# Optimization experiments

Measured on AMD Instinct MI355X. Metric: run time of the kernel, lower is better.

## Reference

```python
import jax, jax.numpy as jnp
import numpy as np

EPS = 1e-6
NUM_HEADS = 16

def _ln(x):
    m = jnp.mean(x, -1, keepdims=True)
    v = jnp.mean((x - m) ** 2, -1, keepdims=True)
    return (x - m) * jax.lax.rsqrt(v + EPS)

def _rms(x, w):
    return x * jax.lax.rsqrt(jnp.mean(x * x, -1, keepdims=True) + EPS) * w

def _to_mha(t):
    B, S, D = t.shape
    return t.reshape(B, S, NUM_HEADS, D // NUM_HEADS).transpose(0, 2, 1, 3)

def _rope(t, freqs):
    # t: [B,H,T,Hd], freqs: [T, Hd//2, 2] (cos, sin)
    B, H, T, Hd = t.shape
    tr = t.reshape(B, H, T, Hd // 2, 2)
    cos, sin = freqs[..., 0], freqs[..., 1]
    r = tr[..., 0] * cos - tr[..., 1] * sin
    i = tr[..., 0] * sin + tr[..., 1] * cos
    return jnp.stack([r, i], -1).reshape(B, H, T, Hd)

def _pre(h, qk_w, qn, kn, v_w, v_b):
    qk = h @ qk_w.T                      # [B,S,2D], no bias (c_qk bias=False)
    q, k = jnp.split(qk, 2, -1)
    q = _rms(_to_mha(q), qn)             # per-head RMSNorm
    k = _rms(_to_mha(k), kn)
    v = _to_mha(h @ v_w.T + v_b)
    return q, k, v

def _post(x, a, pw, pb, w1, b1, w3, b3, w2, b2):
    x = x + a @ pw.T + pb                # residual + c_proj
    h = _ln(x)
    m = (jax.nn.silu(h @ w1.T + b1) * (h @ w3.T + b3)) @ w2.T + b2  # SwiGLU
    return x + m

def _forward(x, c, freqs, px_qk_w, px_qn, px_kn, px_v_w, px_v_b,
             pc_qk_w, pc_qn, pc_kn, pc_v_w, pc_v_b,
             p1_proj_w, p1_proj_b, p1_w1, p1_b1, p1_w3, p1_b3, p1_w2, p1_b2,
             p2_proj_w, p2_proj_b, p2_w1, p2_b1, p2_w3, p2_b3, p2_w2, p2_b2):
    x_ln, c_ln = _ln(x), _ln(c)
    qc, kc, vc = _pre(c_ln, pc_qk_w, pc_qn, pc_kn, pc_v_w, pc_v_b)
    qx, kx, vx = _pre(x_ln, px_qk_w, px_qn, px_kn, px_v_w, px_v_b)
    q = jnp.concatenate([qc, qx], 2)     # [B,H,T,Hd], T = S+L
    k = jnp.concatenate([kc, kx], 2)
    v = jnp.concatenate([vc, vx], 2)
    q = _rope(q, freqs)
    k = _rope(k, freqs)
    Hd = q.shape[-1]
    scores = jnp.einsum('bhqd,bhkd->bhqk', q, k) / jnp.sqrt(jnp.float32(Hd))
    T = scores.shape[-1]
    causal = jnp.tril(jnp.ones((T, T), bool))
    scores = jnp.where(causal, scores, jnp.finfo(scores.dtype).min)
    p = jax.nn.softmax(scores, -1)
    y = jnp.einsum('bhqk,bhkd->bhqd', p, v)
    B, D = x.shape[0], x.shape[-1]
    y = y.transpose(0, 2, 1, 3).reshape(B, -1, D)  # [B,T,D]
    S = c.shape[1]
    y_c, y_x = y[:, :S], y[:, S:]
    x_out = _post(x, y_x, p1_proj_w, p1_proj_b, p1_w1, p1_b1, p1_w3, p1_b3, p1_w2, p1_b2)
    c_out = _post(c, y_c, p2_proj_w, p2_proj_b, p2_w1, p2_b1, p2_w3, p2_b3, p2_w2, p2_b2)
    return x_out, c_out

def setup_inputs() -> dict:
    B, L, S, D, H, FF = 1, 1536, 512, 1024, 16, 4096
    Hd, T = D // H, L + S
    key = jax.random.key(0)
    ks = iter(jax.random.split(key, 40))
    def rn(shape, s=0.02):
        return (jax.random.normal(next(ks), shape, jnp.float32) * s)
    pos = jnp.arange(T, dtype=jnp.float32)
    inv = 1.0 / (10000.0 ** (jnp.arange(0, Hd, 2, dtype=jnp.float32) / Hd))
    ang = pos[:, None] * inv[None, :]
    freqs = jnp.stack([jnp.cos(ang), jnp.sin(ang)], -1)  # [T, Hd//2, 2]
    inp = {
        'x': jax.random.normal(next(ks), (B, L, D), jnp.float32),
        'c': jax.random.normal(next(ks), (B, S, D), jnp.float32),
        'freqs': freqs,
        'px_qk_w': rn((2 * D, D)), 'px_qn': jnp.ones((Hd,)), 'px_kn': jnp.ones((Hd,)),
        'px_v_w': rn((D, D)), 'px_v_b': rn((D,)),
        'pc_qk_w': rn((2 * D, D)), 'pc_qn': jnp.ones((Hd,)), 'pc_kn': jnp.ones((Hd,)),
        'pc_v_w': rn((D, D)), 'pc_v_b': rn((D,)),
    }
    for pfx in ('p1', 'p2'):
        inp[pfx + '_proj_w'] = rn((D, D)); inp[pfx + '_proj_b'] = rn((D,))
        inp[pfx + '_w1'] = rn((FF, D)); inp[pfx + '_b1'] = rn((FF,))
        inp[pfx + '_w3'] = rn((FF, D)); inp[pfx + '_b3'] = rn((FF,))
        inp[pfx + '_w2'] = rn((D, FF)); inp[pfx + '_b2'] = rn((D,))
    return inp

def reference(x, c, freqs, px_qk_w, px_qn, px_kn, px_v_w, px_v_b,
              pc_qk_w, pc_qn, pc_kn, pc_v_w, pc_v_b,
              p1_proj_w, p1_proj_b, p1_w1, p1_b1, p1_w3, p1_b3, p1_w2, p1_b2,
              p2_proj_w, p2_proj_b, p2_w1, p2_b1, p2_w3, p2_b3, p2_w2, p2_b2):
    return _forward(x, c, freqs, px_qk_w, px_qn, px_kn, px_v_w, px_v_b,
                    pc_qk_w, pc_qn, pc_kn, pc_v_w, pc_v_b,
                    p1_proj_w, p1_proj_b, p1_w1, p1_b1, p1_w3, p1_b3, p1_w2, p1_b2,
                    p2_proj_w, p2_proj_b, p2_w1, p2_b1, p2_w3, p2_b3, p2_w2, p2_b2)
```

## Files before the change

### kernel.cpp

```cpp
#include <hip/hip_runtime.h>

typedef __attribute__((ext_vector_type(8))) short short8;
typedef __attribute__((ext_vector_type(4))) float floatx4;

__device__ __forceinline__ float bf2f(unsigned short u) {
  union { unsigned int i; float f; } v; v.i = ((unsigned int)u) << 16; return v.f;
}
__device__ __forceinline__ unsigned short f2bf(float f) {
  union { float f; unsigned int i; } v; v.f = f;
  unsigned int x = v.i + 0x7fffu + ((v.i >> 16) & 1u);
  return (unsigned short)(x >> 16);
}
__device__ __forceinline__ float loadE(const void* p, size_t i, int f) {
  return f ? ((const float*)p)[i] : bf2f(((const unsigned short*)p)[i]);
}
__device__ __forceinline__ uint4 packbf(float4 a, float4 b) {
  union { unsigned short u[8]; uint4 v; } p;
  p.u[0] = f2bf(a.x); p.u[1] = f2bf(a.y); p.u[2] = f2bf(a.z); p.u[3] = f2bf(a.w);
  p.u[4] = f2bf(b.x); p.u[5] = f2bf(b.y); p.u[6] = f2bf(b.z); p.u[7] = f2bf(b.w);
  return p.v;
}

__global__ void detect_kernel(const unsigned int* __restrict__ probe, int* __restrict__ flag) {
  if (threadIdx.x == 0 && blockIdx.x == 0) *flag = (probe[0] == 0x3F800000u) ? 1 : 0;
}

struct CArgs {
  const void* in[12];
  unsigned short* out[12];
  unsigned int cum[12];
};
__global__ __launch_bounds__(256) void convw_kernel(CArgs a, int total_chunks,
                                                    const int* __restrict__ flagp) {
  const int flag = *flagp;
  for (int c = blockIdx.x * 256 + threadIdx.x; c < total_chunks; c += gridDim.x * 256) {
    int s = 0;
    while (c >= (int)a.cum[s]) ++s;
    unsigned int base = s ? a.cum[s - 1] : 0u;
    size_t e = (size_t)(c - base) * 8;
    if (flag) {
      const float* in = (const float*)a.in[s] + e;
      float4 v0 = *(const float4*)in;
      float4 v1 = *(const float4*)(in + 4);
      *(uint4*)(a.out[s] + e) = packbf(v0, v1);
    } else {
      *(uint4*)(a.out[s] + e) = *(const uint4*)((const unsigned short*)a.in[s] + e);
    }
  }
}

__global__ __launch_bounds__(256) void zero_kernel(void* __restrict__ out, int out_elems,
                                                   const int* __restrict__ flagp) {
  int limit = (*flagp) ? (out_elems >> 2) : (out_elems >> 3);
  int i = blockIdx.x * 256 + threadIdx.x;
  if (i < limit) ((uint4*)out)[i] = make_uint4(0, 0, 0, 0);
}

__global__ __launch_bounds__(256) void ln_ext_kernel(const void* __restrict__ cin,
                                                     const void* __restrict__ xin,
                                                     unsigned short* __restrict__ out,
                                                     const int* __restrict__ flagp) {
  const int D = 1024, S = 512;
  const int flag = *flagp;
  int row = blockIdx.x;
  const void* src = (row < S) ? cin : xin;
  size_t rb = (size_t)(row < S ? row : row - S) * D;
  int base = threadIdx.x * 4;
  float x0 = loadE(src, rb + base + 0, flag);
  float x1 = loadE(src, rb + base + 1, flag);
  float x2 = loadE(src, rb + base + 2, flag);
  float x3 = loadE(src, rb + base + 3, flag);
  float s1 = x0 + x1 + x2 + x3;
  float s2 = x0 * x0 + x1 * x1 + x2 * x2 + x3 * x3;
  for (int off = 32; off; off >>= 1) {
    s1 += __shfl_down(s1, off, 64);
    s2 += __shfl_down(s2, off, 64);
  }
  __shared__ float red[8];
  int wid = threadIdx.x >> 6;
  if ((threadIdx.x & 63) == 0) { red[wid] = s1; red[4 + wid] = s2; }
  __syncthreads();
  s1 = red[0] + red[1] + red[2] + red[3];
  s2 = red[4] + red[5] + red[6] + red[7];
  float mean = s1 * (1.0f / D);
  float var = s2 * (1.0f / D) - mean * mean;
  float inv = rsqrtf(var + 1e-6f);
  unsigned short* dst = out + (size_t)row * D + base;
  dst[0] = f2bf((x0 - mean) * inv);
  dst[1] = f2bf((x1 - mean) * inv);
  dst[2] = f2bf((x2 - mean) * inv);
  dst[3] = f2bf((x3 - mean) * inv);
}

__global__ __launch_bounds__(256) void ln_mid_kernel(const unsigned short* __restrict__ in,
                                                     unsigned short* __restrict__ outc,
                                                     unsigned short* __restrict__ outx) {
  const int D = 1024, S = 512;
  int row = blockIdx.x;
  const unsigned short* src = in + (size_t)row * D;
  int base = threadIdx.x * 4;
  float x0 = bf2f(src[base + 0]);
  float x1 = bf2f(src[base + 1]);
  float x2 = bf2f(src[base + 2]);
  float x3 = bf2f(src[base + 3]);
  float s1 = x0 + x1 + x2 + x3;
  float s2 = x0 * x0 + x1 * x1 + x2 * x2 + x3 * x3;
  for (int off = 32; off; off >>= 1) {
    s1 += __shfl_down(s1, off, 64);
    s2 += __shfl_down(s2, off, 64);
  }
  __shared__ float red[8];
  int wid = threadIdx.x >> 6;
  if ((threadIdx.x & 63) == 0) { red[wid] = s1; red[4 + wid] = s2; }
  __syncthreads();
  s1 = red[0] + red[1] + red[2] + red[3];
  s2 = red[4] + red[5] + red[6] + red[7];
  float mean = s1 * (1.0f / D);
  float var = s2 * (1.0f / D) - mean * mean;
  float inv = rsqrtf(var + 1e-6f);
  unsigned short* dst = (row < S ? outc + (size_t)row * D : outx + (size_t)(row - S) * D) + base;
  dst[0] = f2bf((x0 - mean) * inv);
  dst[1] = f2bf((x1 - mean) * inv);
  dst[2] = f2bf((x2 - mean) * inv);
  dst[3] = f2bf((x3 - mean) * inv);
}

struct GArgs {
  const unsigned short* A[4];
  const void* B[4];
  const void* bias[4];
  const void* res[4];
  void* C[4];
  unsigned long long oo[4];
  int mcum[4];
  int N[4];
  int K;
  int nd;
};

#define BAR() asm volatile("s_waitcnt lgkmcnt(0)\n\ts_barrier" ::: "memory")

template <int RES_MODE, int OUT_MODE, int SPLITK, int BBF16>
__global__ __launch_bounds__(256) void gemm_kernel(GArgs g, const int* __restrict__ flagp) {
  const int flag = *flagp;
  int by = blockIdx.y;
  int d = 0;
  while (d < g.nd - 1 && by >= g.mcum[d]) ++d;
  int mbase = (d == 0) ? 0 : g.mcum[d - 1];
  const int m0 = (by - mbase) * 128;
  const int N = g.N[d];
  const int n0 = blockIdx.x * 128;
  if (n0 >= N) return;
  const int K = g.K;
  int kbeg = 0, kend = K;
  if (SPLITK > 1) {
    if (!flag) {
      if (blockIdx.z != 0) return;
    } else {
      int kl = K / SPLITK;
      kbeg = blockIdx.z * kl;
      kend = kbeg + kl;
    }
  }
  const int nt = (kend - kbeg) >> 5;

  __shared__ __align__(16) unsigned short sA[2 * 5120];
  __shared__ __align__(16) unsigned short sB[2 * 5120];

  const int tid = threadIdx.x;
  const int lane = tid & 63;
  const int wave = tid >> 6;
  const int wm = (wave >> 1) * 64, wn = (wave & 1) * 64;
  const int srow = tid >> 2;
  const int scol = (tid & 3) * 8;
  const int wo0 = srow * 40 + scol;
  const int wo1 = wo0 + 64 * 40;
  const unsigned short* Ag0 = g.A[d] + (size_t)(m0 + srow) * K + kbeg + scol;
  const unsigned short* Ag1 = Ag0 + (size_t)64 * K;
  const unsigned short* Bh0 = (const unsigned short*)g.B[d] + (size_t)(n0 + srow) * K + kbeg + scol;
  const unsigned short* Bh1 = Bh0 + (size_t)64 * K;
  const float* Bf0 = (const float*)g.B[d] + (size_t)(n0 + srow) * K + kbeg + scol;
  const float* Bf1 = Bf0 + (size_t)64 * K;

  uint4 ra0, ra1, rb0, rb1;
  auto load_tile = [&](int kk) {
    ra0 = *(const uint4*)(Ag0 + kk);
    ra1 = *(const uint4*)(Ag1 + kk);
    if (BBF16 || !flag) {
      rb0 = *(const uint4*)(Bh0 + kk);
      rb1 = *(const uint4*)(Bh1 + kk);
    } else {
      float4 x0 = *(const float4*)(Bf0 + kk), x1 = *(const float4*)(Bf0 + kk + 4);
      float4 y0 = *(const float4*)(Bf1 + kk), y1 = *(const float4*)(Bf1 + kk + 4);
      rb0 = packbf(x0, x1);
      rb1 = packbf(y0, y1);
    }
  };
  auto store_tile = [&](int buf) {
    unsigned short* sa = sA + buf * 5120;
    unsigned short* sb = sB + buf * 5120;
    *(uint4*)(sa + wo0) = ra0;
    *(uint4*)(sa + wo1) = ra1;
    *(uint4*)(sb + wo0) = rb0;
    *(uint4*)(sb + wo1) = rb1;
  };

  load_tile(0);
  store_tile(0);
  if (nt > 1) load_tile(32);
  BAR();

  const int fr = lane & 15, fc = (lane >> 4) * 8;
  floatx4 acc[4][4] = {};
  for (int t = 0; t < nt; ++t) {
    if (t + 1 < nt) {
      store_tile((t + 1) & 1);
      if (t + 2 < nt) load_tile((t + 2) * 32);
    }
    const unsigned short* as = sA + (t & 1) * 5120;
    const unsigned short* bs = sB + (t & 1) * 5120;
    short8 af[4], bfr[4];
    #pragma unroll
    for (int i = 0; i < 4; ++i) {
      af[i]  = *(const short8*)(as + (wm + i * 16 + fr) * 40 + fc);
      bfr[i] = *(const short8*)(bs + (wn + i * 16 + fr) * 40 + fc);
    }
    #pragma unroll
    for (int mi = 0; mi < 4; ++mi)
      #pragma unroll
      for (int ni = 0; ni < 4; ++ni)
        acc[mi][ni] = __builtin_amdgcn_mfma_f32_16x16x32_bf16(af[mi], bfr[ni], acc[mi][ni], 0, 0, 0);
    if (t + 1 < nt) BAR();
  }

  const void* bias = g.bias[d];
  const void* res = g.res[d];
  void* C = g.C[d];
  const size_t oo = g.oo[d];
  const bool first = (SPLITK <= 1) || (blockIdx.z == 0) || !flag;
  #pragma unroll
  for (int mi = 0; mi < 4; ++mi)
    #pragma unroll
    for (int ni = 0; ni < 4; ++ni)
      #pragma unroll
      for (int r = 0; r < 4; ++r) {
        int row = m0 + wm + mi * 16 + (lane >> 4) * 4 + r;
        int col = n0 + wn + ni * 16 + (lane & 15);
        float val = acc[mi][ni][r];
        size_t off = (size_t)row * N + col;
        if (first) {
          if (bias) val += loadE(bias, (size_t)col, flag);
          if (RES_MODE == 1) val += loadE(res, off, flag);
          if (RES_MODE == 3) {
            float h1v = bf2f(((const unsigned short*)res)[off]);
            val = (h1v / (1.0f + __expf(-h1v))) * val;
          }
          if (RES_MODE == 4) val += bf2f(((const unsigned short*)res)[off]);
        }
        if (OUT_MODE == 0) {
          ((unsigned short*)C)[off] = f2bf(val);
        } else {
          if (flag) {
            if (SPLITK > 1) atomicAdd((float*)C + oo + off, val);
            else            ((float*)C)[oo + off] = val;
          } else {
            ((unsigned short*)C)[oo + off] = f2bf(val);
          }
        }
      }
}

__global__ __launch_bounds__(256) void rmsrope_kernel(
    unsigned short* __restrict__ qk,
    const void* __restrict__ qn_c, const void* __restrict__ kn_c,
    const void* __restrict__ qn_x, const void* __restrict__ kn_x,
    const void* __restrict__ freqs, const int* __restrict__ flagp) {
  const int flag = *flagp;
  int t = blockIdx.x;
  int h = blockIdx.y * 4 + (threadIdx.x >> 6);
  int d = threadIdx.x & 63;
  unsigned short* qrow = qk + (size_t)t * 2048 + h * 64;
  unsigned short* krow = qrow + 1024;
  float q = bf2f(qrow[d]), k = bf2f(krow[d]);
  float qs = q * q, ks = k * k;
  for (int off = 32; off; off >>= 1) {
    qs += __shfl_xor(qs, off, 64);
    ks += __shfl_xor(ks, off, 64);
  }
  const void* qn = (t < 512) ? qn_c : qn_x;
  const void* kn = (t < 512) ? kn_c : kn_x;
  q = q * rsqrtf(qs * (1.0f / 64.0f) + 1e-6f) * loadE(qn, d, flag);
  k = k * rsqrtf(ks * (1.0f / 64.0f) + 1e-6f) * loadE(kn, d, flag);
  int j = d >> 1;
  float cv = loadE(freqs, (size_t)(t * 32 + j) * 2 + 0, flag);
  float sv = loadE(freqs, (size_t)(t * 32 + j) * 2 + 1, flag);
  float qo = __shfl_xor(q, 1, 64);
  float ko = __shfl_xor(k, 1, 64);
  float qn2, kn2;
  if ((d & 1) == 0) { qn2 = q * cv - qo * sv; kn2 = k * cv - ko * sv; }
  else              { qn2 = qo * sv + q * cv; kn2 = ko * sv + k * cv; }
  qrow[d] = f2bf(qn2);
  krow[d] = f2bf(kn2);
}

__global__ __launch_bounds__(256) void attn_kernel(const unsigned short* __restrict__ qk,
                                                   const unsigned short* __restrict__ v,
                                                   unsigned short* __restrict__ y) {
  int id = blockIdx.x;
  int blk = (id & 256) ? (31 - (id & 31)) : (id & 31);
  int h = (id >> 5) & 15;
  int wv = threadIdx.x >> 6;
  int lane = threadIdx.x & 63;
  int qbase = blk * 64 + wv * 16;

  __shared__ __align__(16) unsigned short Ks[64 * 72];
  __shared__ __align__(16) unsigned short Vt[64 * 64];
  __shared__ __align__(16) unsigned short ps[4][16 * 72];

  short8 qa[2];
  {
    int m = lane & 15, dj = (lane >> 4) * 8;
    const unsigned short* qp = qk + (size_t)(qbase + m) * 2048 + h * 64 + dj;
    qa[0] = *(const short8*)(qp);
    qa[1] = *(const short8*)(qp + 32);
  }
  floatx4 o[4] = {};
  float mrow[4] = {-1e30f, -1e30f, -1e30f, -1e30f};
  float lrow[4] = {0.f, 0.f, 0.f, 0.f};
  int ntiles = blk + 1;
  for (int tile = 0; tile < ntiles; ++tile) {
    int j0 = tile * 64;
    __syncthreads();
    for (int c2 = threadIdx.x; c2 < 512; c2 += 256) {
      int key = c2 >> 3, d0 = (c2 & 7) * 8;
      *(short8*)(Ks + key * 72 + d0) =
          *(const short8*)(qk + (size_t)(j0 + key) * 2048 + 1024 + h * 64 + d0);
      short8 vv = *(const short8*)(v + (size_t)(j0 + key) * 1024 + h * 64 + d0);
      int bphys = ((key >> 3) ^ (d0 >> 3)) * 8 + (key & 7);
      #pragma unroll
      for (int jj = 0; jj < 8; ++jj)
        Vt[(d0 + jj) * 64 + bphys] = ((const unsigned short*)&vv)[jj];
    }
    __syncthreads();
    floatx4 sacc[4];
    #pragma unroll
    for (int kg = 0; kg < 4; ++kg) {
      floatx4 z = {0.f, 0.f, 0.f, 0.f};
      #pragma unroll
      for (int kc = 0; kc < 2; ++kc) {
        short8 kb = *(const short8*)(Ks + (kg * 16 + (lane & 15)) * 72 + kc * 32 + (lane >> 4) * 8);
        z = __builtin_amdgcn_mfma_f32_16x16x32_bf16(qa[kc], kb, z, 0, 0, 0);
      }
      sacc[kg] = z;
    }
    #pragma unroll
    for (int kg = 0; kg < 4; ++kg)
      #pragma unroll
      for (int r = 0; r < 4; ++r) {
        int key_g = j0 + kg * 16 + (lane & 15);
        int q_g = qbase + (lane >> 4) * 4 + r;
        float s = sacc[kg][r] * 0.125f;
        sacc[kg][r] = (key_g <= q_g) ? s : -1e30f;
      }
    #pragma unroll
    for (int r = 0; r < 4; ++r) {
      float mx = fmaxf(fmaxf(sacc[0][r], sacc[1][r]), fmaxf(sacc[2][r], sacc[3][r]));
      mx = fmaxf(mx, __shfl_xor(mx, 1, 64));
      mx = fmaxf(mx, __shfl_xor(mx, 2, 64));
      mx = fmaxf(mx, __shfl_xor(mx, 4, 64));
      mx = fmaxf(mx, __shfl_xor(mx, 8, 64));
      float mnew = fmaxf(mrow[r], mx);
      float al = __expf(mrow[r] - mnew);
      mrow[r] = mnew;
      float sum = 0.f;
      #pragma unroll
      for (int kg = 0; kg < 4; ++kg) {
        float p = __expf(sacc[kg][r] - mnew);
        sacc[kg][r] = p;
        sum += p;
      }
      sum += __shfl_xor(sum, 1, 64);
      sum += __shfl_xor(sum, 2, 64);
      sum += __shfl_xor(sum, 4, 64);
      sum += __shfl_xor(sum, 8, 64);
      lrow[r] = lrow[r] * al + sum;
      #pragma unroll
      for (int ni = 0; ni < 4; ++ni) o[ni][r] *= al;
    }
    unsigned short* pw = ps[wv];
    #pragma unroll
    for (int kg = 0; kg < 4; ++kg)
      #pragma unroll
      for (int r = 0; r < 4; ++r)
        pw[((lane >> 4) * 4 + r) * 72 + kg * 16 + (lane & 15)] = f2bf(sacc[kg][r]);
    asm volatile("s_waitcnt lgkmcnt(0)" ::: "memory");
    short8 pa[2];
    pa[0] = *(const short8*)(pw + (lane & 15) * 72 + (lane >> 4) * 8);
    pa[1] = *(const short8*)(pw + (lane & 15) * 72 + 32 + (lane >> 4) * 8);
    #pragma unroll
    for (int ni = 0; ni < 4; ++ni) {
      floatx4 z = o[ni];
      int dd = ni * 16 + (lane & 15);
      #pragma unroll
      for (int kc = 0; kc < 2; ++kc) {
        int bphys = (kc * 4 + (lane >> 4)) ^ (dd >> 3);
        short8 vb = *(const short8*)(Vt + dd * 64 + bphys * 8);
        z = __builtin_amdgcn_mfma_f32_16x16x32_bf16(pa[kc], vb, z, 0, 0, 0);
      }
      o[ni] = z;
    }
  }
  #pragma unroll
  for (int ni = 0; ni < 4; ++ni)
    #pragma unroll
    for (int r = 0; r < 4; ++r) {
      int q = qbase + (lane >> 4) * 4 + r;
      int dd = ni * 16 + (lane & 15);
      y[(size_t)q * 1024 + h * 64 + dd] = f2bf(o[ni][r] / lrow[r]);
    }
}

extern "C" void kernel_launch(void* const* d_in, const int* in_sizes, int n_in,
                              void* d_out, int out_size, void* d_ws, size_t ws_size,
                              hipStream_t stream) {
  const int L = 1536, S = 512, D = 1024, T = 2048, FF = 4096;
  const void* x        = d_in[0];
  const void* c        = d_in[1];
  const void* freqs    = d_in[2];
  const void* px_qk_w  = d_in[3];
  const void* px_qn    = d_in[4];
  const void* px_kn    = d_in[5];
  const void* px_v_w   = d_in[6];
  const void* px_v_b   = d_in[7];
  const void* pc_qk_w  = d_in[8];
  const void* pc_qn    = d_in[9];
  const void* pc_kn    = d_in[10];
  const void* pc_v_w   = d_in[11];
  const void* pc_v_b   = d_in[12];
  const void* p1_proj_w = d_in[13];
  const void* p1_proj_b = d_in[14];
  const void* p1_w1 = d_in[15];
  const void* p1_b1 = d_in[16];
  const void* p1_w3 = d_in[17];
  const void* p1_b3 = d_in[18];
  const void* p1_w2 = d_in[19];
  const void* p1_b2 = d_in[20];
  const void* p2_proj_w = d_in[21];
  const void* p2_proj_b = d_in[22];
  const void* p2_w1 = d_in[23];
  const void* p2_b1 = d_in[24];
  const void* p2_w3 = d_in[25];
  const void* p2_b3 = d_in[26];
  const void* p2_w2 = d_in[27];
  const void* p2_b2 = d_in[28];

  char* ws = (char*)d_ws;
  unsigned short* hln     = (unsigned short*)(ws);
  unsigned short* ybuf    = (unsigned short*)(ws);
  unsigned short* h1c     = (unsigned short*)(ws);
  unsigned short* qkbuf   = (unsigned short*)(ws + ((size_t)4  << 20));
  unsigned short* h1x     = (unsigned short*)(ws + ((size_t)4  << 20));
  unsigned short* vbuf    = (unsigned short*)(ws + ((size_t)12 << 20));
  unsigned short* mid     = (unsigned short*)(ws + ((size_t)16 << 20));
  unsigned short* midln_c = (unsigned short*)(ws + ((size_t)20 << 20));
  int*            flag    = (int*)(ws + ((size_t)21 << 20));
  unsigned short* midln_x = (unsigned short*)d_out;
  unsigned short* hlnx    = hln + (size_t)S * D;

  const bool conv = ws_size >= ((size_t)90 << 20);
  unsigned short* wbf = (unsigned short*)(ws + ((size_t)24 << 20));
  unsigned short* b_qk_c = wbf + 0;
  unsigned short* b_qk_x = wbf + 2097152;
  unsigned short* b_v_c  = wbf + 4194304;
  unsigned short* b_v_x  = wbf + 5242880;
  unsigned short* b_pj1  = wbf + 6291456;
  unsigned short* b_pj2  = wbf + 7340032;
  unsigned short* b_w1p1 = wbf + 8388608;
  unsigned short* b_w1p2 = wbf + 12582912;
  unsigned short* b_w3p1 = wbf + 16777216;
  unsigned short* b_w3p2 = wbf + 20971520;
  unsigned short* b_w2p1 = wbf + 25165824;
  unsigned short* b_w2p2 = wbf + 29360128;

  detect_kernel<<<1, 64, 0, stream>>>((const unsigned int*)px_qn, flag);

  if (conv) {
    CArgs ca;
    const void* ins[12]   = {pc_qk_w, px_qk_w, pc_v_w, px_v_w, p1_proj_w, p2_proj_w,
                             p1_w1, p2_w1, p1_w3, p2_w3, p1_w2, p2_w2};
    unsigned short* os[12] = {b_qk_c, b_qk_x, b_v_c, b_v_x, b_pj1, b_pj2,
                              b_w1p1, b_w1p2, b_w3p1, b_w3p2, b_w2p1, b_w2p2};
    unsigned int cnt[12]  = {262144, 262144, 131072, 131072, 131072, 131072,
                             524288, 524288, 524288, 524288, 524288, 524288};
    unsigned int cum = 0;
    for (int i = 0; i < 12; ++i) { ca.in[i] = ins[i]; ca.out[i] = os[i]; cum += cnt[i]; ca.cum[i] = cum; }
    convw_kernel<<<2048, 256, 0, stream>>>(ca, (int)cum, flag);
  }

  ln_ext_kernel<<<T, 256, 0, stream>>>(c, x, hln, flag);

  {
    GArgs g = {};
    g.A[0] = hln;  g.bias[0] = nullptr; g.C[0] = qkbuf;                    g.mcum[0] = 4;  g.N[0] = 2048;
    g.A[1] = hlnx; g.bias[1] = nullptr; g.C[1] = qkbuf + (size_t)S * 2048; g.mcum[1] = 16; g.N[1] = 2048;
    g.A[2] = hln;  g.bias[2] = pc_v_b;  g.C[2] = vbuf;                     g.mcum[2] = 20; g.N[2] = 1024;
    g.A[3] = hlnx; g.bias[3] = px_v_b;  g.C[3] = vbuf + (size_t)S * D;     g.mcum[3] = 32; g.N[3] = 1024;
    g.K = 1024; g.nd = 4;
    if (conv) {
      g.B[0] = b_qk_c; g.B[1] = b_qk_x; g.B[2] = b_v_c; g.B[3] = b_v_x;
      gemm_kernel<0, 0, 1, 1><<<dim3(16, 32), 256, 0, stream>>>(g, flag);
    } else {
      g.B[0] = pc_qk_w; g.B[1] = px_qk_w; g.B[2] = pc_v_w; g.B[3] = px_v_w;
      gemm_kernel<0, 0, 1, 0><<<dim3(16, 32), 256, 0, stream>>>(g, flag);
    }
  }
  rmsrope_kernel<<<dim3(T, 4), 256, 0, stream>>>(qkbuf, pc_qn, pc_kn, px_qn, px_kn, freqs, flag);
  attn_kernel<<<512, 256, 0, stream>>>(qkbuf, vbuf, ybuf);

  {
    GArgs g = {};
    g.A[0] = ybuf;                  g.bias[0] = p2_proj_b; g.res[0] = c; g.C[0] = mid;                  g.mcum[0] = 4;  g.N[0] = 1024;
    g.A[1] = ybuf + (size_t)S * D;  g.bias[1] = p1_proj_b; g.res[1] = x; g.C[1] = mid + (size_t)S * D;  g.mcum[1] = 16; g.N[1] = 1024;
    g.K = 1024; g.nd = 2;
    if (conv) {
      g.B[0] = b_pj2; g.B[1] = b_pj1;
      gemm_kernel<1, 0, 1, 1><<<dim3(8, 16), 256, 0, stream>>>(g, flag);
    } else {
      g.B[0] = p2_proj_w; g.B[1] = p1_proj_w;
      gemm_kernel<1, 0, 1, 0><<<dim3(8, 16), 256, 0, stream>>>(g, flag);
    }
  }
  ln_mid_kernel<<<T, 256, 0, stream>>>(mid, midln_c, midln_x);

  {
    GArgs g = {};
    g.A[0] = midln_x; g.bias[0] = p1_b1; g.C[0] = h1x; g.mcum[0] = 12; g.N[0] = 4096;
    g.A[1] = midln_c; g.bias[1] = p2_b1; g.C[1] = h1c; g.mcum[1] = 16; g.N[1] = 4096;
    g.K = 1024; g.nd = 2;
    if (conv) {
      g.B[0] = b_w1p1; g.B[1] = b_w1p2;
      gemm_kernel<0, 0, 1, 1><<<dim3(32, 16), 256, 0, stream>>>(g, flag);
    } else {
      g.B[0] = p1_w1; g.B[1] = p2_w1;
      gemm_kernel<0, 0, 1, 0><<<dim3(32, 16), 256, 0, stream>>>(g, flag);
    }
  }
  {
    GArgs g = {};
    g.A[0] = midln_x; g.bias[0] = p1_b3; g.res[0] = h1x; g.C[0] = h1x; g.mcum[0] = 12; g.N[0] = 4096;
    g.A[1] = midln_c; g.bias[1] = p2_b3; g.res[1] = h1c; g.C[1] = h1c; g.mcum[1] = 16; g.N[1] = 4096;
    g.K = 1024; g.nd = 2;
    if (conv) {
      g.B[0] = b_w3p1; g.B[1] = b_w3p2;
      gemm_kernel<3, 0, 1, 1><<<dim3(32, 16), 256, 0, stream>>>(g, flag);
    } else {
      g.B[0] = p1_w3; g.B[1] = p2_w3;
      gemm_kernel<3, 0, 1, 0><<<dim3(32, 16), 256, 0, stream>>>(g, flag);
    }
  }
  zero_kernel<<<2048, 256, 0, stream>>>(d_out, out_size, flag);
  {
    GArgs g = {};
    g.A[0] = h1x; g.bias[0] = p1_b2; g.res[0] = mid + (size_t)S * D; g.C[0] = d_out; g.oo[0] = 0;             g.mcum[0] = 12; g.N[0] = 1024;
    g.A[1] = h1c; g.bias[1] = p2_b2; g.res[1] = mid;                 g.C[1] = d_out; g.oo[1] = (size_t)L * D; g.mcum[1] = 16; g.N[1] = 1024;
    g.K = 4096; g.nd = 2;
    if (conv) {
      g.B[0] = b_w2p1; g.B[1] = b_w2p2;
      gemm_kernel<4, 2, 4, 1><<<dim3(8, 16, 4), 256, 0, stream>>>(g, flag);
    } else {
      g.B[0] = p1_w2; g.B[1] = p2_w2;
      gemm_kernel<4, 2, 4, 0><<<dim3(8, 16, 4), 256, 0, stream>>>(g, flag);
    }
  }
}
```

Baseline: 532.0 us.

## Use direct global-to-LDS loads in bf16 GEMM and replace split-K atomics with reduce

For GEMMs whose B operand is already bf16, tiles are now loaded with global_load_lds straight into a swizzled, unpadded LDS layout, skipping the register staging step. The loop waits on vmcnt before each barrier instead of keeping loads in flight in registers. The final split-K W2 GEMM now writes per-split fp32 partials to workspace, and a new reduce kernel sums them and adds bias and residual. This removes the zeroing pass and the atomics but adds extra partial-buffer traffic and one more launch.

```diff
diff --git a/kernel.cpp b/kernel.cpp
--- a/kernel.cpp
+++ b/kernel.cpp
@@ -19,6 +19,12 @@
   p.u[0] = f2bf(a.x); p.u[1] = f2bf(a.y); p.u[2] = f2bf(a.z); p.u[3] = f2bf(a.w);
   p.u[4] = f2bf(b.x); p.u[5] = f2bf(b.y); p.u[6] = f2bf(b.z); p.u[7] = f2bf(b.w);
   return p.v;
+}
+
+__device__ __forceinline__ void gl16(const unsigned short* g, unsigned short* l) {
+  __builtin_amdgcn_global_load_lds(
+      (const __attribute__((address_space(1))) void*)g,
+      (__attribute__((address_space(3))) void*)l, 16, 0, 0);
 }
 
 __global__ void detect_kernel(const unsigned int* __restrict__ probe, int* __restrict__ flag) {
@@ -56,6 +62,34 @@
   if (i < limit) ((uint4*)out)[i] = make_uint4(0, 0, 0, 0);
 }
 
+__global__ __launch_bounds__(256) void reduce_kernel(const float* __restrict__ part,
+                                                     const unsigned short* __restrict__ mid,
+                                                     const void* __restrict__ b1,
+                                                     const void* __restrict__ b2,
+                                                     float* __restrict__ out,
+                                                     const int* __restrict__ flagp) {
+  if (!*flagp) return;
+  const size_t TD = 2097152, LD = (size_t)1536 * 1024, SD = (size_t)512 * 1024;
+  size_t i = ((size_t)blockIdx.x * 256 + threadIdx.x) * 4;
+  if (i >= TD) return;
+  float4 v  = *(const float4*)(part + i);
+  float4 v1 = *(const float4*)(part + TD + i);
+  float4 v2 = *(const float4*)(part + 2 * TD + i);
+  float4 v3 = *(const float4*)(part + 3 * TD + i);
+  v.x += v1.x + v2.x + v3.x;
+  v.y += v1.y + v2.y + v3.y;
+  v.z += v1.z + v2.z + v3.z;
+  v.w += v1.w + v2.w + v3.w;
+  int col = (int)(i & 1023);
+  const float* bias = (const float*)((i < LD) ? b1 : b2);
+  size_t ri = (i < LD) ? (SD + i) : (i - LD);
+  v.x += bias[col + 0] + bf2f(mid[ri + 0]);
+  v.y += bias[col + 1] + bf2f(mid[ri + 1]);
+  v.z += bias[col + 2] + bf2f(mid[ri + 2]);
+  v.w += bias[col + 3] + bf2f(mid[ri + 3]);
+  *(float4*)(out + i) = v;
+}
+
 __global__ __launch_bounds__(256) void ln_ext_kernel(const void* __restrict__ cin,
                                                      const void* __restrict__ xin,
                                                      unsigned short* __restrict__ out,
@@ -136,9 +170,11 @@
   int N[4];
   int K;
   int nd;
+  float* part;
 };
 
 #define BAR() asm volatile("s_waitcnt lgkmcnt(0)\n\ts_barrier" ::: "memory")
+#define FBAR() asm volatile("s_waitcnt vmcnt(0) lgkmcnt(0)\n\ts_barrier" ::: "memory")
 
 template <int RES_MODE, int OUT_MODE, int SPLITK, int BBF16>
 __global__ __launch_bounds__(256) void gemm_kernel(GArgs g, const int* __restrict__ flagp) {
@@ -164,73 +200,97 @@
   }
   const int nt = (kend - kbeg) >> 5;
 
-  __shared__ __align__(16) unsigned short sA[2 * 5120];
-  __shared__ __align__(16) unsigned short sB[2 * 5120];
+  constexpr int BSTRIDE = BBF16 ? 4096 : 5120;
+  __shared__ __align__(16) unsigned short sA[2 * BSTRIDE];
+  __shared__ __align__(16) unsigned short sB[2 * BSTRIDE];
 
   const int tid = threadIdx.x;
   const int lane = tid & 63;
   const int wave = tid >> 6;
   const int wm = (wave >> 1) * 64, wn = (wave & 1) * 64;
   const int srow = tid >> 2;
-  const int scol = (tid & 3) * 8;
-  const int wo0 = srow * 40 + scol;
-  const int wo1 = wo0 + 64 * 40;
+  const int scol = BBF16 ? ((((tid & 3) ^ ((tid >> 3) & 3))) * 8) : ((tid & 3) * 8);
   const unsigned short* Ag0 = g.A[d] + (size_t)(m0 + srow) * K + kbeg + scol;
   const unsigned short* Ag1 = Ag0 + (size_t)64 * K;
   const unsigned short* Bh0 = (const unsigned short*)g.B[d] + (size_t)(n0 + srow) * K + kbeg + scol;
   const unsigned short* Bh1 = Bh0 + (size_t)64 * K;
-  const float* Bf0 = (const float*)g.B[d] + (size_t)(n0 + srow) * K + kbeg + scol;
-  const float* Bf1 = Bf0 + (size_t)64 * K;
-
-  uint4 ra0, ra1, rb0, rb1;
-  auto load_tile = [&](int kk) {
-    ra0 = *(const uint4*)(Ag0 + kk);
-    ra1 = *(const uint4*)(Ag1 + kk);
-    if (BBF16 || !flag) {
-      rb0 = *(const uint4*)(Bh0 + kk);
-      rb1 = *(const uint4*)(Bh1 + kk);
-    } else {
-      float4 x0 = *(const float4*)(Bf0 + kk), x1 = *(const float4*)(Bf0 + kk + 4);
-      float4 y0 = *(const float4*)(Bf1 + kk), y1 = *(const float4*)(Bf1 + kk + 4);
-      rb0 = packbf(x0, x1);
-      rb1 = packbf(y0, y1);
-    }
-  };
-  auto store_tile = [&](int buf) {
-    unsigned short* sa = sA + buf * 5120;
-    unsigned short* sb = sB + buf * 5120;
-    *(uint4*)(sa + wo0) = ra0;
-    *(uint4*)(sa + wo1) = ra1;
-    *(uint4*)(sb + wo0) = rb0;
-    *(uint4*)(sb + wo1) = rb1;
-  };
-
-  load_tile(0);
-  store_tile(0);
-  if (nt > 1) load_tile(32);
-  BAR();
-
-  const int fr = lane & 15, fc = (lane >> 4) * 8;
+
+  const int fr = lane & 15;
+  const int rdo = BBF16 ? ((((lane >> 4) ^ ((fr >> 1) & 3))) * 8) : ((lane >> 4) * 8);
+  constexpr int PITCH = BBF16 ? 32 : 40;
   floatx4 acc[4][4] = {};
-  for (int t = 0; t < nt; ++t) {
-    if (t + 1 < nt) {
-      store_tile((t + 1) & 1);
-      if (t + 2 < nt) load_tile((t + 2) * 32);
-    }
-    const unsigned short* as = sA + (t & 1) * 5120;
-    const unsigned short* bs = sB + (t & 1) * 5120;
+  auto compute = [&](const unsigned short* as, const unsigned short* bs) {
     short8 af[4], bfr[4];
     #pragma unroll
     for (int i = 0; i < 4; ++i) {
-      af[i]  = *(const short8*)(as + (wm + i * 16 + fr) * 40 + fc);
-      bfr[i] = *(const short8*)(bs + (wn + i * 16 + fr) * 40 + fc);
+      af[i]  = *(const short8*)(as + (wm + i * 16 + fr) * PITCH + rdo);
+      bfr[i] = *(const short8*)(bs + (wn + i * 16 + fr) * PITCH + rdo);
     }
     #pragma unroll
     for (int mi = 0; mi < 4; ++mi)
       #pragma unroll
       for (int ni = 0; ni < 4; ++ni)
         acc[mi][ni] = __builtin_amdgcn_mfma_f32_16x16x32_bf16(af[mi], bfr[ni], acc[mi][ni], 0, 0, 0);
-    if (t + 1 < nt) BAR();
+  };
+
+  if (BBF16) {
+    unsigned short* lA0 = sA + wave * 512;
+    unsigned short* lA1 = lA0 + 2048;
+    unsigned short* lB0 = sB + wave * 512;
+    unsigned short* lB1 = lB0 + 2048;
+    auto stage = [&](int buf, int kk) {
+      int bo = buf * 4096;
+      gl16(Ag0 + kk, lA0 + bo);
+      gl16(Ag1 + kk, lA1 + bo);
+      gl16(Bh0 + kk, lB0 + bo);
+      gl16(Bh1 + kk, lB1 + bo);
+    };
+    stage(0, 0);
+    FBAR();
+    for (int t = 0; t < nt; ++t) {
+      if (t + 1 < nt) stage((t + 1) & 1, (t + 1) * 32);
+      compute(sA + (t & 1) * 4096, sB + (t & 1) * 4096);
+      if (t + 1 < nt) FBAR();
+    }
+  } else {
+    const float* Bf0 = (const float*)g.B[d] + (size_t)(n0 + srow) * K + kbeg + scol;
+    const float* Bf1 = Bf0 + (size_t)64 * K;
+    const int wo0 = srow * 40 + scol;
+    const int wo1 = wo0 + 64 * 40;
+    uint4 ra0, ra1, rb0, rb1;
+    auto load_tile = [&](int kk) {
+      ra0 = *(const uint4*)(Ag0 + kk);
+      ra1 = *(const uint4*)(Ag1 + kk);
+      if (!flag) {
+        rb0 = *(const uint4*)(Bh0 + kk);
+        rb1 = *(const uint4*)(Bh1 + kk);
+      } else {
+        float4 x0 = *(const float4*)(Bf0 + kk), x1 = *(const float4*)(Bf0 + kk + 4);
+        float4 y0 = *(const float4*)(Bf1 + kk), y1 = *(const float4*)(Bf1 + kk + 4);
+        rb0 = packbf(x0, x1);
+        rb1 = packbf(y0, y1);
+      }
+    };
+    auto store_tile = [&](int buf) {
+      unsigned short* sa = sA + buf * 5120;
+      unsigned short* sb = sB + buf * 5120;
+      *(uint4*)(sa + wo0) = ra0;
+      *(uint4*)(sa + wo1) = ra1;
+      *(uint4*)(sb + wo0) = rb0;
+      *(uint4*)(sb + wo1) = rb1;
+    };
+    load_tile(0);
+    store_tile(0);
+    if (nt > 1) load_tile(32);
+    BAR();
+    for (int t = 0; t < nt; ++t) {
+      if (t + 1 < nt) {
+        store_tile((t + 1) & 1);
+        if (t + 2 < nt) load_tile((t + 2) * 32);
+      }
+      compute(sA + (t & 1) * 5120, sB + (t & 1) * 5120);
+      if (t + 1 < nt) BAR();
+    }
   }
 
   const void* bias = g.bias[d];
@@ -238,6 +298,7 @@
   void* C = g.C[d];
   const size_t oo = g.oo[d];
   const bool first = (SPLITK <= 1) || (blockIdx.z == 0) || !flag;
+  const bool rawpart = (OUT_MODE == 3) && (flag != 0);
   #pragma unroll
   for (int mi = 0; mi < 4; ++mi)
     #pragma unroll
@@ -248,7 +309,7 @@
         int col = n0 + wn + ni * 16 + (lane & 15);
         float val = acc[mi][ni][r];
         size_t off = (size_t)row * N + col;
-        if (first) {
+        if (first && !rawpart) {
           if (bias) val += loadE(bias, (size_t)col, flag);
           if (RES_MODE == 1) val += loadE(res, off, flag);
           if (RES_MODE == 3) {
@@ -259,6 +320,9 @@
         }
         if (OUT_MODE == 0) {
           ((unsigned short*)C)[off] = f2bf(val);
+        } else if (OUT_MODE == 3) {
+          if (flag) g.part[(size_t)blockIdx.z * 2097152 + oo + off] = val;
+          else      ((unsigned short*)C)[oo + off] = f2bf(val);
         } else {
           if (flag) {
             if (SPLITK > 1) atomicAdd((float*)C + oo + off, val);
@@ -481,6 +545,7 @@
   unsigned short* b_w3p2 = wbf + 20971520;
   unsigned short* b_w2p1 = wbf + 25165824;
   unsigned short* b_w2p2 = wbf + 29360128;
+  float* part = (float*)(ws + ((size_t)40 << 20));
 
   detect_kernel<<<1, 64, 0, stream>>>((const unsigned int*)px_qn, flag);
 
@@ -558,18 +623,22 @@
       gemm_kernel<3, 0, 1, 0><<<dim3(32, 16), 256, 0, stream>>>(g, flag);
     }
   }
-  zero_kernel<<<2048, 256, 0, stream>>>(d_out, out_size, flag);
-  {
+  if (conv) {
     GArgs g = {};
     g.A[0] = h1x; g.bias[0] = p1_b2; g.res[0] = mid + (size_t)S * D; g.C[0] = d_out; g.oo[0] = 0;             g.mcum[0] = 12; g.N[0] = 1024;
     g.A[1] = h1c; g.bias[1] = p2_b2; g.res[1] = mid;                 g.C[1] = d_out; g.oo[1] = (size_t)L * D; g.mcum[1] = 16; g.N[1] = 1024;
     g.K = 4096; g.nd = 2;
-    if (conv) {
-      g.B[0] = b_w2p1; g.B[1] = b_w2p2;
-      gemm_kernel<4, 2, 4, 1><<<dim3(8, 16, 4), 256, 0, stream>>>(g, flag);
-    } else {
-      g.B[0] = p1_w2; g.B[1] = p2_w2;
-      gemm_kernel<4, 2, 4, 0><<<dim3(8, 16, 4), 256, 0, stream>>>(g, flag);
-    }
-  }
-}
+    g.part = part;
+    g.B[0] = b_w2p1; g.B[1] = b_w2p2;
+    gemm_kernel<4, 3, 4, 1><<<dim3(8, 16, 4), 256, 0, stream>>>(g, flag);
+    reduce_kernel<<<2048, 256, 0, stream>>>(part, mid, p1_b2, p2_b2, (float*)d_out, flag);
+  } else {
+    zero_kernel<<<2048, 256, 0, stream>>>(d_out, out_size, flag);
+    GArgs g = {};
+    g.A[0] = h1x; g.bias[0] = p1_b2; g.res[0] = mid + (size_t)S * D; g.C[0] = d_out; g.oo[0] = 0;             g.mcum[0] = 12; g.N[0] = 1024;
+    g.A[1] = h1c; g.bias[1] = p2_b2; g.res[1] = mid;                 g.C[1] = d_out; g.oo[1] = (size_t)L * D; g.mcum[1] = 16; g.N[1] = 1024;
+    g.K = 4096; g.nd = 2;
+    g.B[0] = p1_w2; g.B[1] = p2_w2;
+    gemm_kernel<4, 2, 4, 0><<<dim3(8, 16, 4), 256, 0, stream>>>(g, flag);
+  }
+}
```

After: 511.8 us. -3.8%, faster.
